# Kernel optimization log

Hardware: AMD Instinct MI355X
Metric: run time of the kernel (lower is better)

Reference implementation:

```python
import jax, jax.numpy as jnp
import numpy as np

EPS = 0.05
ITERS = 3
NORM_EPS = 1e-12  # torch F.normalize clamp


def setup_inputs() -> dict:
    key = jax.random.key(0)
    k1, k2, k3, k4 = jax.random.split(key, 4)
    x = jax.random.normal(k1, (16, 768, 64, 64), jnp.float32)
    conv_w = jax.random.normal(k2, (256, 768), jnp.float32) * 0.02  # 1x1 conv kernel [out,in]
    conv_b = jax.random.normal(k3, (256,), jnp.float32) * 0.02
    v = jax.random.normal(k4, (32, 256), jnp.float32)  # [num_clusters, token_dim]
    return {"x": x, "conv_w": conv_w, "conv_b": conv_b, "v": v}


def _l2_normalize(a, axis=-1):
    n = jnp.sqrt(jnp.sum(a * a, axis=axis, keepdims=True))
    return a / jnp.maximum(n, NORM_EPS)


def _log_optimal_transport(scores):
    # scores: [b, m, n]; log-domain Sinkhorn with uniform marginals
    b, m, n = scores.shape
    norm = -jnp.log(jnp.float32(m + n))
    Z = scores / EPS
    u = jnp.full((b, m), 0.0, Z.dtype)
    v = jnp.full((b, n), 0.0, Z.dtype)
    for _ in range(ITERS):
        u = norm - jax.scipy.special.logsumexp(Z + v[:, None, :], axis=2)
        v = norm - jax.scipy.special.logsumexp(Z + u[:, :, None], axis=1)
    return jnp.exp(Z + u[:, :, None] + v[:, None, :] - norm)


def reference(x, conv_w, conv_b, v):
    # 1x1 conv projection: [b, C, H, W] -> [b, D, H, W]
    xp = jnp.einsum('bchw,dc->bdhw', x, conv_w) + conv_b[None, :, None, None]
    b, d, H, W = xp.shape
    x_proj = xp.reshape(b, d, H * W).transpose(0, 2, 1)  # [b, hw, d]
    xf = _l2_normalize(x_proj)  # l2_normalize branch
    w = _l2_normalize(v)        # cluster weights normalized (in-place copy in torch)
    scores = jnp.einsum('bnd,md->bnm', xf, w)  # [b, hw, m]
    weights = _log_optimal_transport(scores.transpose(0, 2, 1)).transpose(0, 2, 1)  # [b, hw, m]
    v_tilde = jnp.einsum('bnd,bnm->bmd', xf, weights)  # [b, m, d]
    return (v_tilde, x_proj)
```

## Files before the change

### kernel.cpp

```cpp
#include <hip/hip_runtime.h>
#include <math.h>

#define NORM_C (-8.3255483f)

typedef __attribute__((ext_vector_type(8))) short bf16x8;
typedef __attribute__((ext_vector_type(4))) float f32x4;

union U8 { uint4 q; unsigned u[4]; bf16x8 v; };

__device__ inline unsigned short f2bf_rne(float f) {
    unsigned u = __float_as_uint(f);
    unsigned r = u + 0x7fffu + ((u >> 16) & 1u);
    return (unsigned short)(r >> 16);
}
__device__ inline unsigned pack_bf2(float lo, float hi) {
    unsigned a = __float_as_uint(lo) + 0x8000u;
    unsigned b = __float_as_uint(hi) + 0x8000u;
    return __builtin_amdgcn_perm(b, a, 0x07060302u);
}

__global__ __launch_bounds__(64) void w_prep(const float* __restrict__ W,
                                             const float* __restrict__ v_in,
                                             unsigned short* __restrict__ Wb,
                                             unsigned short* __restrict__ wnb) {
    const int bx = blockIdx.x, tid = threadIdx.x;
    if (bx < 768) {
        int i = (bx * 64 + tid) * 4;
        float4 w = *(const float4*)(W + i);
        unsigned lo = (unsigned)f2bf_rne(w.x) | ((unsigned)f2bf_rne(w.y) << 16);
        unsigned hi = (unsigned)f2bf_rne(w.z) | ((unsigned)f2bf_rne(w.w) << 16);
        *(uint2*)(Wb + i) = make_uint2(lo, hi);
    } else {
        int row = bx - 768;
        float4 v = *(const float4*)(v_in + row * 256 + tid * 4);
        float s = v.x * v.x + v.y * v.y + v.z * v.z + v.w * v.w;
#pragma unroll
        for (int off = 32; off > 0; off >>= 1) s += __shfl_xor(s, off);
        float inv = 1.0f / fmaxf(sqrtf(s), 1e-12f);
        unsigned lo = (unsigned)f2bf_rne(v.x * inv) | ((unsigned)f2bf_rne(v.y * inv) << 16);
        unsigned hi = (unsigned)f2bf_rne(v.z * inv) | ((unsigned)f2bf_rne(v.w * inv) << 16);
        *(uint2*)(wnb + row * 256 + tid * 4) = make_uint2(lo, hi);
    }
}

__global__ __launch_bounds__(256) void conv_mega(const float* __restrict__ x,
                                                 const unsigned short* __restrict__ Wb,
                                                 const float* __restrict__ bias,
                                                 const unsigned short* __restrict__ wnb,
                                                 float* __restrict__ xp,
                                                 float* __restrict__ inv_norm,
                                                 float* __restrict__ Z,
                                                 float2* __restrict__ u1p) {
    __shared__ unsigned Bs[2][128 * 17];
    __shared__ float ssq_s[128];
    __shared__ float invs_s[128];
    __shared__ unsigned xfs[128 * 33];
    __shared__ float2 upart_s[4][32];

    const int tid = threadIdx.x;
    const int lane = tid & 63;
    const int wid = tid >> 6;
    const int wn = wid & 1, wd = wid >> 1;
    const int b = blockIdx.y;
    const int n0 = blockIdx.x * 128;
    const int l15 = lane & 15, l4 = lane >> 4;
    const float* xb = x + (size_t)b * 768 * 4096;

    f32x4 acc[8][4];
#pragma unroll
    for (int i = 0; i < 8; ++i)
#pragma unroll
        for (int j = 0; j < 4; ++j) acc[i][j] = (f32x4){0.f, 0.f, 0.f, 0.f};

    const int n2 = tid & 63;
    const float* xpt = xb + n0 + 2 * n2;
    float2 ga[4], gb[4];

    auto LOADX = [&](int k0) {
#pragma unroll
        for (int i = 0; i < 4; ++i) {
            const float* p = xpt + (size_t)(k0 + 2 * (wid + 4 * i)) * 4096;
            ga[i] = *(const float2*)p;
            gb[i] = *(const float2*)(p + 4096);
        }
    };
    auto STOREB = [&](int buf) {
#pragma unroll
        for (int i = 0; i < 4; ++i) {
            int ch = wid + 4 * i;
            Bs[buf][(2 * n2) * 17 + ch]     = pack_bf2(ga[i].x, gb[i].x);
            Bs[buf][(2 * n2 + 1) * 17 + ch] = pack_bf2(ga[i].y, gb[i].y);
        }
    };

    LOADX(0);
    STOREB(0);
    __syncthreads();
    int cur = 0;
    for (int k0 = 0; k0 < 768; k0 += 32) {
        if (k0 + 32 < 768) LOADX(k0 + 32);

        U8 af[8];
#pragma unroll
        for (int dt = 0; dt < 8; ++dt) {
            int row = wd * 128 + dt * 16 + l15;
            af[dt].q = *(const uint4*)(Wb + (size_t)row * 768 + k0 + l4 * 8);
        }
#pragma unroll
        for (int nt = 0; nt < 4; ++nt) {
            int col = wn * 64 + nt * 16 + l15;
            int base = col * 17 + l4 * 4;
            U8 bf;
            bf.u[0] = Bs[cur][base];     bf.u[1] = Bs[cur][base + 1];
            bf.u[2] = Bs[cur][base + 2]; bf.u[3] = Bs[cur][base + 3];
#pragma unroll
            for (int dt = 0; dt < 8; ++dt)
                acc[dt][nt] = __builtin_amdgcn_mfma_f32_16x16x32_bf16(
                    af[dt].v, bf.v, acc[dt][nt], 0, 0, 0);
        }
        if (k0 + 32 < 768) STOREB(cur ^ 1);
        __syncthreads();
        cur ^= 1;
    }

    float ssq[4] = {0.f, 0.f, 0.f, 0.f};
#pragma unroll
    for (int dt = 0; dt < 8; ++dt) {
        int d = wd * 128 + dt * 16 + l4 * 4;
        float4 bi = *(const float4*)(bias + d);
#pragma unroll
        for (int nt = 0; nt < 4; ++nt) {
            int n = n0 + wn * 64 + nt * 16 + l15;
            f32x4 o = acc[dt][nt];
            o.x += bi.x; o.y += bi.y; o.z += bi.z; o.w += bi.w;
            acc[dt][nt] = o;
            *(f32x4*)(xp + ((size_t)(b * 4096 + n)) * 256 + d) = o;
            ssq[nt] += o.x * o.x + o.y * o.y + o.z * o.z + o.w * o.w;
        }
    }
#pragma unroll
    for (int nt = 0; nt < 4; ++nt) {
        ssq[nt] += __shfl_xor(ssq[nt], 16);
        ssq[nt] += __shfl_xor(ssq[nt], 32);
    }
    if (wd == 0 && l4 == 0) {
#pragma unroll
        for (int nt = 0; nt < 4; ++nt) ssq_s[wn * 64 + nt * 16 + l15] = ssq[nt];
    }
    __syncthreads();
    if (wd == 1 && l4 == 0) {
#pragma unroll
        for (int nt = 0; nt < 4; ++nt) {
            int nl = wn * 64 + nt * 16 + l15;
            float inv = 1.0f / fmaxf(sqrtf(ssq[nt] + ssq_s[nl]), 1e-12f);
            invs_s[nl] = inv;
            inv_norm[b * 4096 + n0 + nl] = inv;
        }
    }

    f32x4 accz[2][2];
#pragma unroll
    for (int i = 0; i < 2; ++i)
#pragma unroll
        for (int j = 0; j < 2; ++j) accz[i][j] = (f32x4){0.f, 0.f, 0.f, 0.f};

    for (int q = 0; q < 4; ++q) {
        __syncthreads();
        if (wd == (q >> 1)) {
#pragma unroll
            for (int dt4 = 0; dt4 < 4; ++dt4) {
                int dt = (q & 1) * 4 + dt4;
#pragma unroll
                for (int nt = 0; nt < 4; ++nt) {
                    int n = wn * 64 + nt * 16 + l15;
                    float inv = invs_s[n];
                    f32x4 a = acc[dt][nt];
                    int base = n * 33 + dt4 * 8 + l4 * 2;
                    xfs[base]     = pack_bf2(a.x * inv, a.y * inv);
                    xfs[base + 1] = pack_bf2(a.z * inv, a.w * inv);
                }
            }
        }
        __syncthreads();
#pragma unroll
        for (int s = 0; s < 2; ++s) {
            U8 wf[2];
#pragma unroll
            for (int mt = 0; mt < 2; ++mt)
                wf[mt].q = *(const uint4*)(wnb + (mt * 16 + l15) * 256 +
                                           q * 64 + s * 32 + l4 * 8);
#pragma unroll
            for (int sti = 0; sti < 2; ++sti) {
                int st = wid + sti * 4;
                int arow = (st * 16 + l15) * 33 + s * 16 + l4 * 4;
                U8 af;
                af.u[0] = xfs[arow]; af.u[1] = xfs[arow + 1];
                af.u[2] = xfs[arow + 2]; af.u[3] = xfs[arow + 3];
#pragma unroll
                for (int mt = 0; mt < 2; ++mt)
                    accz[sti][mt] = __builtin_amdgcn_mfma_f32_16x16x32_bf16(
                        af.v, wf[mt].v, accz[sti][mt], 0, 0, 0);
            }
        }
    }
#pragma unroll
    for (int sti = 0; sti < 2; ++sti)
#pragma unroll
        for (int mt = 0; mt < 2; ++mt) {
            accz[sti][mt].x *= 20.f; accz[sti][mt].y *= 20.f;
            accz[sti][mt].z *= 20.f; accz[sti][mt].w *= 20.f;
            int m = mt * 16 + l15;
            int st = wid + sti * 4;
            *(f32x4*)&Z[((size_t)(b * 32 + m)) * 4096 + n0 + st * 16 + l4 * 4] =
                accz[sti][mt];
        }
#pragma unroll
    for (int mt = 0; mt < 2; ++mt) {
        float v0[8] = {accz[0][mt].x, accz[0][mt].y, accz[0][mt].z, accz[0][mt].w,
                       accz[1][mt].x, accz[1][mt].y, accz[1][mt].z, accz[1][mt].w};
        float mx = v0[0];
#pragma unroll
        for (int i = 1; i < 8; ++i) mx = fmaxf(mx, v0[i]);
        float s = 0.f;
#pragma unroll
        for (int i = 0; i < 8; ++i) s += __expf(v0[i] - mx);
#pragma unroll
        for (int off = 16; off < 64; off <<= 1) {
            float omx = __shfl_xor(mx, off);
            float os = __shfl_xor(s, off);
            float nm = fmaxf(mx, omx);
            s = s * __expf(mx - nm) + os * __expf(omx - nm);
            mx = nm;
        }
        if (lane < 16) upart_s[wid][mt * 16 + lane] = make_float2(mx, s);
    }
    __syncthreads();
    if (wid == 0 && lane < 32) {
        float2 p = upart_s[0][lane];
        float mx = p.x, s = p.y;
#pragma unroll
        for (int w = 1; w < 4; ++w) {
            float2 qq = upart_s[w][lane];
            float nm = fmaxf(mx, qq.x);
            s = s * __expf(mx - nm) + qq.y * __expf(qq.x - nm);
            mx = nm;
        }
        u1p[((size_t)b * 32 + blockIdx.x) * 32 + lane] = make_float2(mx, s);
    }
}

template <int NIN>
__global__ __launch_bounds__(256) void sink_step(const float* __restrict__ Z,
                                                 const float2* __restrict__ up_in,
                                                 float2* __restrict__ up_out) {
    __shared__ float u_s[32];
    __shared__ float2 red_s[4][32];
    const int tid = threadIdx.x;
    const int lane = tid & 63, wid = tid >> 6;
    const int b = blockIdx.y;
    const int chunk = blockIdx.x;
    const int n = chunk * 256 + tid;

    if (tid < 32) {
        float2 p = up_in[((size_t)b * NIN) * 32 + tid];
        float mx = p.x, s = p.y;
#pragma unroll 4
        for (int t = 1; t < NIN; ++t) {
            float2 q = up_in[((size_t)b * NIN + t) * 32 + tid];
            float nm = fmaxf(mx, q.x);
            s = s * __expf(mx - nm) + q.y * __expf(q.x - nm);
            mx = nm;
        }
        u_s[tid] = NORM_C - (mx + __logf(s));
    }
    __syncthreads();

    float z[32];
#pragma unroll
    for (int m = 0; m < 32; ++m) z[m] = Z[((size_t)(b * 32 + m)) * 4096 + n];

    float mx = z[0] + u_s[0];
#pragma unroll
    for (int m = 1; m < 32; ++m) mx = fmaxf(mx, z[m] + u_s[m]);
    float s = 0.f;
#pragma unroll
    for (int m = 0; m < 32; ++m) s += __expf(z[m] + u_s[m] - mx);
    float vv = NORM_C - (mx + __logf(s));

#pragma unroll
    for (int m = 0; m < 32; ++m) {
        float val = z[m] + vv;
        float vmx = val;
#pragma unroll
        for (int off = 1; off < 64; off <<= 1) vmx = fmaxf(vmx, __shfl_xor(vmx, off));
        float e = __expf(val - vmx);
#pragma unroll
        for (int off = 1; off < 64; off <<= 1) e += __shfl_xor(e, off);
        if (lane == 0) red_s[wid][m] = make_float2(vmx, e);
    }
    __syncthreads();
    if (tid < 32) {
        float2 p = red_s[0][tid];
        float gm = p.x, gs = p.y;
#pragma unroll
        for (int w = 1; w < 4; ++w) {
            float2 q = red_s[w][tid];
            float nm = fmaxf(gm, q.x);
            gs = gs * __expf(gm - nm) + q.y * __expf(q.x - nm);
            gm = nm;
        }
        up_out[((size_t)b * 16 + chunk) * 32 + tid] = make_float2(gm, gs);
    }
}

__global__ __launch_bounds__(256) void vtilde_part_k(const float* __restrict__ xp,
                                                     const float* __restrict__ inv_norm,
                                                     const float* __restrict__ Z,
                                                     const float2* __restrict__ u3p,
                                                     float* __restrict__ part) {
    __shared__ float u_s[32];
    __shared__ float v3_s[256];
    __shared__ float inv_s[256];
    __shared__ float z_s[32 * 257];
    __shared__ float wt[64 * 36];
    const int tid = threadIdx.x;
    const int cx = blockIdx.x;
    const int chunk = cx >> 1, dh = cx & 1;
    const int b = blockIdx.y;
    const int n0 = chunk * 256;

    if (tid < 32) {
        float2 p = u3p[((size_t)b * 16) * 32 + tid];
        float gm = p.x, gs = p.y;
#pragma unroll
        for (int t = 1; t < 16; ++t) {
            float2 q = u3p[((size_t)b * 16 + t) * 32 + tid];
            float nm = fmaxf(gm, q.x);
            gs = gs * __expf(gm - nm) + q.y * __expf(q.x - nm);
            gm = nm;
        }
        u_s[tid] = NORM_C - (gm + __logf(gs));
    }
    __syncthreads();
    {
        int n = n0 + tid;
        float zr[32];
#pragma unroll
        for (int m = 0; m < 32; ++m) {
            zr[m] = Z[((size_t)(b * 32 + m)) * 4096 + n];
            z_s[m * 257 + tid] = zr[m];
        }
        float mx = zr[0] + u_s[0];
#pragma unroll
        for (int m = 1; m < 32; ++m) mx = fmaxf(mx, zr[m] + u_s[m]);
        float s = 0.f;
#pragma unroll
        for (int m = 0; m < 32; ++m) s += __expf(zr[m] + u_s[m] - mx);
        v3_s[tid] = NORM_C - (mx + __logf(s));
        inv_s[tid] = inv_norm[b * 4096 + n];
    }
    __syncthreads();

    const int dg = tid & 31, mq = tid >> 5;
    f32x4 acc[4];
#pragma unroll
    for (int j = 0; j < 4; ++j) acc[j] = (f32x4){0.f, 0.f, 0.f, 0.f};
    const float* xpb = xp + ((size_t)(b * 4096 + n0)) * 256 + dh * 128 + dg * 4;

    for (int t = 0; t < 4; ++t) {
#pragma unroll
        for (int i = 0; i < 8; ++i) {
            int e = tid + i * 256;
            int mW = e >> 6, nn = e & 63;
            int nl = t * 64 + nn;
            wt[nn * 36 + mW] =
                __expf(z_s[mW * 257 + nl] + u_s[mW] + v3_s[nl] - NORM_C) * inv_s[nl];
        }
        __syncthreads();
#pragma unroll 4
        for (int nn = 0; nn < 64; ++nn) {
            float4 xv = *(const float4*)(xpb + (size_t)(t * 64 + nn) * 256);
            float4 wv = *(const float4*)&wt[nn * 36 + mq * 4];
            acc[0].x += wv.x * xv.x; acc[0].y += wv.x * xv.y; acc[0].z += wv.x * xv.z; acc[0].w += wv.x * xv.w;
            acc[1].x += wv.y * xv.x; acc[1].y += wv.y * xv.y; acc[1].z += wv.y * xv.z; acc[1].w += wv.y * xv.w;
            acc[2].x += wv.z * xv.x; acc[2].y += wv.z * xv.y; acc[2].z += wv.z * xv.z; acc[2].w += wv.z * xv.w;
            acc[3].x += wv.w * xv.x; acc[3].y += wv.w * xv.y; acc[3].z += wv.w * xv.z; acc[3].w += wv.w * xv.w;
        }
        __syncthreads();
    }
#pragma unroll
    for (int j = 0; j < 4; ++j) {
        int m = mq * 4 + j;
        *(f32x4*)&part[((size_t)(b * 16 + chunk)) * 8192 + m * 256 + dh * 128 + dg * 4] = acc[j];
    }
}

__global__ __launch_bounds__(256) void vtilde_reduce(const float* __restrict__ part,
                                                     float* __restrict__ out_vt) {
    int o = blockIdx.x * 256 + threadIdx.x;
    int b = o >> 13, r = o & 8191;
    float s = 0.f;
#pragma unroll
    for (int c = 0; c < 16; ++c)
        s += part[((size_t)(b * 16 + c)) * 8192 + r];
    out_vt[o] = s;
}

extern "C" void kernel_launch(void* const* d_in, const int* in_sizes, int n_in,
                              void* d_out, int out_size, void* d_ws, size_t ws_size,
                              hipStream_t stream) {
    const float* x      = (const float*)d_in[0];
    const float* conv_w = (const float*)d_in[1];
    const float* conv_b = (const float*)d_in[2];
    const float* v_in   = (const float*)d_in[3];

    float* out_vt = (float*)d_out;
    float* out_xp = (float*)d_out + 131072;

    float* ws = (float*)d_ws;
    float*          inv_norm = ws;
    unsigned short* Wb       = (unsigned short*)(ws + 65536);
    unsigned short* wnb      = (unsigned short*)(ws + 163840);
    float*          Zbuf     = ws + 167936;
    float2*         u1p      = (float2*)(ws + 2265088);
    float2*         u2p      = (float2*)(ws + 2297856);
    float2*         u3p      = (float2*)(ws + 2314240);
    float*          part     = ws + 2330624;

    w_prep<<<800, 64, 0, stream>>>(conv_w, v_in, Wb, wnb);
    conv_mega<<<dim3(32, 16), 256, 0, stream>>>(x, Wb, conv_b, wnb, out_xp,
                                                inv_norm, Zbuf, u1p);
    sink_step<32><<<dim3(16, 16), 256, 0, stream>>>(Zbuf, u1p, u2p);
    sink_step<16><<<dim3(16, 16), 256, 0, stream>>>(Zbuf, u2p, u3p);
    vtilde_part_k<<<dim3(32, 16), 256, 0, stream>>>(out_xp, inv_norm, Zbuf, u3p, part);
    vtilde_reduce<<<512, 256, 0, stream>>>(part, out_vt);
}
```

Before: 414.9 us.

## Halve conv tile width, pre-tile bf16 weights, double grid for occupancy

The fused conv kernel now processes 64 pixels per block instead of 128, which doubles the grid to 1024 blocks and sets launch bounds for 4 blocks per CU, so fewer accumulators are held per thread. The weight prep writes conv weights in a K-tiled layout so each MFMA A-fragment load is contiguous. The K loop is unrolled by two with separate register sets for the prefetch. The sink_step and workspace layout are updated for 64 partial logsumexp entries per batch. Smaller tiles reuse each loaded weight fragment across fewer pixels, so the kernel reads more weight data in total in exchange for better latency hiding.

```diff
diff --git a/kernel.cpp b/kernel.cpp
--- a/kernel.cpp
+++ b/kernel.cpp
@@ -21,15 +21,18 @@
 
 __global__ __launch_bounds__(64) void w_prep(const float* __restrict__ W,
                                              const float* __restrict__ v_in,
-                                             unsigned short* __restrict__ Wb,
+                                             unsigned short* __restrict__ Wbt,
                                              unsigned short* __restrict__ wnb) {
     const int bx = blockIdx.x, tid = threadIdx.x;
     if (bx < 768) {
         int i = (bx * 64 + tid) * 4;
+        int row = i / 768;
+        int k = i - row * 768;
+        int t = k >> 5, q = (k >> 3) & 3, e = k & 7;
         float4 w = *(const float4*)(W + i);
         unsigned lo = (unsigned)f2bf_rne(w.x) | ((unsigned)f2bf_rne(w.y) << 16);
         unsigned hi = (unsigned)f2bf_rne(w.z) | ((unsigned)f2bf_rne(w.w) << 16);
-        *(uint2*)(Wb + i) = make_uint2(lo, hi);
+        *(uint2*)(Wbt + ((t * 256 + row) << 5) + q * 8 + e) = make_uint2(lo, hi);
     } else {
         int row = bx - 768;
         float4 v = *(const float4*)(v_in + row * 256 + tid * 4);
@@ -43,94 +46,113 @@
     }
 }
 
-__global__ __launch_bounds__(256) void conv_mega(const float* __restrict__ x,
-                                                 const unsigned short* __restrict__ Wb,
-                                                 const float* __restrict__ bias,
-                                                 const unsigned short* __restrict__ wnb,
-                                                 float* __restrict__ xp,
-                                                 float* __restrict__ inv_norm,
-                                                 float* __restrict__ Z,
-                                                 float2* __restrict__ u1p) {
-    __shared__ unsigned Bs[2][128 * 17];
-    __shared__ float ssq_s[128];
-    __shared__ float invs_s[128];
-    __shared__ unsigned xfs[128 * 33];
+__global__ __launch_bounds__(256, 4) void conv_mega(const float* __restrict__ x,
+                                                    const unsigned short* __restrict__ Wbt,
+                                                    const float* __restrict__ bias,
+                                                    const unsigned short* __restrict__ wnb,
+                                                    float* __restrict__ xp,
+                                                    float* __restrict__ inv_norm,
+                                                    float* __restrict__ Z,
+                                                    float2* __restrict__ u1p) {
+    __shared__ unsigned Bs[2][64 * 17];
+    __shared__ unsigned xf_s[64 * 65];
+    __shared__ float ssq_s[4][64];
+    __shared__ float invs_s[64];
     __shared__ float2 upart_s[4][32];
 
     const int tid = threadIdx.x;
     const int lane = tid & 63;
     const int wid = tid >> 6;
-    const int wn = wid & 1, wd = wid >> 1;
     const int b = blockIdx.y;
-    const int n0 = blockIdx.x * 128;
+    const int n0 = blockIdx.x * 64;
     const int l15 = lane & 15, l4 = lane >> 4;
     const float* xb = x + (size_t)b * 768 * 4096;
 
-    f32x4 acc[8][4];
-#pragma unroll
-    for (int i = 0; i < 8; ++i)
+    f32x4 acc[4][4];
+#pragma unroll
+    for (int i = 0; i < 4; ++i)
 #pragma unroll
         for (int j = 0; j < 4; ++j) acc[i][j] = (f32x4){0.f, 0.f, 0.f, 0.f};
 
-    const int n2 = tid & 63;
+    const int n2 = tid & 31, c8 = tid >> 5;
     const float* xpt = xb + n0 + 2 * n2;
-    float2 ga[4], gb[4];
-
-    auto LOADX = [&](int k0) {
-#pragma unroll
-        for (int i = 0; i < 4; ++i) {
-            const float* p = xpt + (size_t)(k0 + 2 * (wid + 4 * i)) * 4096;
-            ga[i] = *(const float2*)p;
-            gb[i] = *(const float2*)(p + 4096);
+
+    float2 gaA[2], gbA[2], gaB[2], gbB[2];
+
+    auto LOADA = [&](int k0) {
+#pragma unroll
+        for (int i = 0; i < 2; ++i) {
+            const float* p = xpt + (size_t)(k0 + 2 * (c8 + 8 * i)) * 4096;
+            gaA[i] = *(const float2*)p;
+            gbA[i] = *(const float2*)(p + 4096);
+        }
+    };
+    auto LOADB = [&](int k0) {
+#pragma unroll
+        for (int i = 0; i < 2; ++i) {
+            const float* p = xpt + (size_t)(k0 + 2 * (c8 + 8 * i)) * 4096;
+            gaB[i] = *(const float2*)p;
+            gbB[i] = *(const float2*)(p + 4096);
+        }
+    };
+    auto STOREA = [&](int buf) {
+#pragma unroll
+        for (int i = 0; i < 2; ++i) {
+            int ch = c8 + 8 * i;
+            Bs[buf][(2 * n2) * 17 + ch]     = pack_bf2(gaA[i].x, gbA[i].x);
+            Bs[buf][(2 * n2 + 1) * 17 + ch] = pack_bf2(gaA[i].y, gbA[i].y);
         }
     };
     auto STOREB = [&](int buf) {
 #pragma unroll
-        for (int i = 0; i < 4; ++i) {
-            int ch = wid + 4 * i;
-            Bs[buf][(2 * n2) * 17 + ch]     = pack_bf2(ga[i].x, gb[i].x);
-            Bs[buf][(2 * n2 + 1) * 17 + ch] = pack_bf2(ga[i].y, gb[i].y);
+        for (int i = 0; i < 2; ++i) {
+            int ch = c8 + 8 * i;
+            Bs[buf][(2 * n2) * 17 + ch]     = pack_bf2(gaB[i].x, gbB[i].x);
+            Bs[buf][(2 * n2 + 1) * 17 + ch] = pack_bf2(gaB[i].y, gbB[i].y);
         }
     };
-
-    LOADX(0);
-    STOREB(0);
-    __syncthreads();
-    int cur = 0;
-    for (int k0 = 0; k0 < 768; k0 += 32) {
-        if (k0 + 32 < 768) LOADX(k0 + 32);
-
-        U8 af[8];
-#pragma unroll
-        for (int dt = 0; dt < 8; ++dt) {
-            int row = wd * 128 + dt * 16 + l15;
-            af[dt].q = *(const uint4*)(Wb + (size_t)row * 768 + k0 + l4 * 8);
-        }
+    auto MFMA_STEP = [&](int t, int buf) {
+        U8 af[4];
+#pragma unroll
+        for (int dt = 0; dt < 4; ++dt)
+            af[dt].q = *(const uint4*)(Wbt +
+                ((t * 256 + wid * 64 + dt * 16 + l15) << 5) + l4 * 8);
 #pragma unroll
         for (int nt = 0; nt < 4; ++nt) {
-            int col = wn * 64 + nt * 16 + l15;
-            int base = col * 17 + l4 * 4;
+            int base = (nt * 16 + l15) * 17 + l4 * 4;
             U8 bf;
-            bf.u[0] = Bs[cur][base];     bf.u[1] = Bs[cur][base + 1];
-            bf.u[2] = Bs[cur][base + 2]; bf.u[3] = Bs[cur][base + 3];
-#pragma unroll
-            for (int dt = 0; dt < 8; ++dt)
+            bf.u[0] = Bs[buf][base];     bf.u[1] = Bs[buf][base + 1];
+            bf.u[2] = Bs[buf][base + 2]; bf.u[3] = Bs[buf][base + 3];
+#pragma unroll
+            for (int dt = 0; dt < 4; ++dt)
                 acc[dt][nt] = __builtin_amdgcn_mfma_f32_16x16x32_bf16(
                     af[dt].v, bf.v, acc[dt][nt], 0, 0, 0);
         }
-        if (k0 + 32 < 768) STOREB(cur ^ 1);
-        __syncthreads();
-        cur ^= 1;
+    };
+
+    LOADA(0);
+    STOREA(0);
+    LOADB(32);
+    __syncthreads();
+    for (int t = 0; t < 24; t += 2) {
+        if (t + 2 < 24) LOADA((t + 2) * 32);
+        MFMA_STEP(t, 0);
+        STOREB(1);
+        __syncthreads();
+        if (t + 3 < 24) LOADB((t + 3) * 32);
+        MFMA_STEP(t + 1, 1);
+        if (t + 2 < 24) STOREA(0);
+        __syncthreads();
     }
 
     float ssq[4] = {0.f, 0.f, 0.f, 0.f};
 #pragma unroll
-    for (int dt = 0; dt < 8; ++dt) {
-        int d = wd * 128 + dt * 16 + l4 * 4;
+    for (int dt = 0; dt < 4; ++dt) {
+        int d = wid * 64 + dt * 16 + l4 * 4;
         float4 bi = *(const float4*)(bias + d);
 #pragma unroll
         for (int nt = 0; nt < 4; ++nt) {
-            int n = n0 + wn * 64 + nt * 16 + l15;
+            int n = n0 + nt * 16 + l15;
             f32x4 o = acc[dt][nt];
             o.x += bi.x; o.y += bi.y; o.z += bi.z; o.w += bi.w;
             acc[dt][nt] = o;
@@ -143,87 +165,70 @@
         ssq[nt] += __shfl_xor(ssq[nt], 16);
         ssq[nt] += __shfl_xor(ssq[nt], 32);
     }
-    if (wd == 0 && l4 == 0) {
-#pragma unroll
-        for (int nt = 0; nt < 4; ++nt) ssq_s[wn * 64 + nt * 16 + l15] = ssq[nt];
-    }
-    __syncthreads();
-    if (wd == 1 && l4 == 0) {
-#pragma unroll
-        for (int nt = 0; nt < 4; ++nt) {
-            int nl = wn * 64 + nt * 16 + l15;
-            float inv = 1.0f / fmaxf(sqrtf(ssq[nt] + ssq_s[nl]), 1e-12f);
-            invs_s[nl] = inv;
-            inv_norm[b * 4096 + n0 + nl] = inv;
-        }
-    }
-
-    f32x4 accz[2][2];
-#pragma unroll
-    for (int i = 0; i < 2; ++i)
-#pragma unroll
-        for (int j = 0; j < 2; ++j) accz[i][j] = (f32x4){0.f, 0.f, 0.f, 0.f};
-
-    for (int q = 0; q < 4; ++q) {
-        __syncthreads();
-        if (wd == (q >> 1)) {
-#pragma unroll
-            for (int dt4 = 0; dt4 < 4; ++dt4) {
-                int dt = (q & 1) * 4 + dt4;
+    if (l4 == 0) {
+#pragma unroll
+        for (int nt = 0; nt < 4; ++nt) ssq_s[wid][nt * 16 + l15] = ssq[nt];
+    }
+    __syncthreads();
+    if (tid < 64) {
+        float s = ssq_s[0][tid] + ssq_s[1][tid] + ssq_s[2][tid] + ssq_s[3][tid];
+        float inv = 1.0f / fmaxf(sqrtf(s), 1e-12f);
+        invs_s[tid] = inv;
+        inv_norm[b * 4096 + n0 + tid] = inv;
+    }
+
+    f32x4 accz[2];
+    accz[0] = (f32x4){0.f, 0.f, 0.f, 0.f};
+    accz[1] = (f32x4){0.f, 0.f, 0.f, 0.f};
+
+    for (int h = 0; h < 2; ++h) {
+        __syncthreads();
+        if ((wid >> 1) == h) {
+            int qh = wid & 1;
+#pragma unroll
+            for (int dt = 0; dt < 4; ++dt)
 #pragma unroll
                 for (int nt = 0; nt < 4; ++nt) {
-                    int n = wn * 64 + nt * 16 + l15;
+                    int n = nt * 16 + l15;
                     float inv = invs_s[n];
                     f32x4 a = acc[dt][nt];
-                    int base = n * 33 + dt4 * 8 + l4 * 2;
-                    xfs[base]     = pack_bf2(a.x * inv, a.y * inv);
-                    xfs[base + 1] = pack_bf2(a.z * inv, a.w * inv);
+                    int base = n * 65 + qh * 32 + dt * 8 + l4 * 2;
+                    xf_s[base]     = pack_bf2(a.x * inv, a.y * inv);
+                    xf_s[base + 1] = pack_bf2(a.z * inv, a.w * inv);
                 }
-            }
-        }
-        __syncthreads();
-#pragma unroll
-        for (int s = 0; s < 2; ++s) {
+        }
+        __syncthreads();
+#pragma unroll
+        for (int s = 0; s < 4; ++s) {
             U8 wf[2];
 #pragma unroll
             for (int mt = 0; mt < 2; ++mt)
                 wf[mt].q = *(const uint4*)(wnb + (mt * 16 + l15) * 256 +
-                                           q * 64 + s * 32 + l4 * 8);
-#pragma unroll
-            for (int sti = 0; sti < 2; ++sti) {
-                int st = wid + sti * 4;
-                int arow = (st * 16 + l15) * 33 + s * 16 + l4 * 4;
-                U8 af;
-                af.u[0] = xfs[arow]; af.u[1] = xfs[arow + 1];
-                af.u[2] = xfs[arow + 2]; af.u[3] = xfs[arow + 3];
-#pragma unroll
-                for (int mt = 0; mt < 2; ++mt)
-                    accz[sti][mt] = __builtin_amdgcn_mfma_f32_16x16x32_bf16(
-                        af.v, wf[mt].v, accz[sti][mt], 0, 0, 0);
-            }
-        }
-    }
-#pragma unroll
-    for (int sti = 0; sti < 2; ++sti)
-#pragma unroll
-        for (int mt = 0; mt < 2; ++mt) {
-            accz[sti][mt].x *= 20.f; accz[sti][mt].y *= 20.f;
-            accz[sti][mt].z *= 20.f; accz[sti][mt].w *= 20.f;
-            int m = mt * 16 + l15;
-            int st = wid + sti * 4;
-            *(f32x4*)&Z[((size_t)(b * 32 + m)) * 4096 + n0 + st * 16 + l4 * 4] =
-                accz[sti][mt];
-        }
+                                           h * 128 + s * 32 + l4 * 8);
+            int arow = (wid * 16 + l15) * 65 + s * 16 + l4 * 4;
+            U8 af2;
+            af2.u[0] = xf_s[arow];     af2.u[1] = xf_s[arow + 1];
+            af2.u[2] = xf_s[arow + 2]; af2.u[3] = xf_s[arow + 3];
+#pragma unroll
+            for (int mt = 0; mt < 2; ++mt)
+                accz[mt] = __builtin_amdgcn_mfma_f32_16x16x32_bf16(
+                    af2.v, wf[mt].v, accz[mt], 0, 0, 0);
+        }
+    }
 #pragma unroll
     for (int mt = 0; mt < 2; ++mt) {
-        float v0[8] = {accz[0][mt].x, accz[0][mt].y, accz[0][mt].z, accz[0][mt].w,
-                       accz[1][mt].x, accz[1][mt].y, accz[1][mt].z, accz[1][mt].w};
-        float mx = v0[0];
-#pragma unroll
-        for (int i = 1; i < 8; ++i) mx = fmaxf(mx, v0[i]);
-        float s = 0.f;
-#pragma unroll
-        for (int i = 0; i < 8; ++i) s += __expf(v0[i] - mx);
+        accz[mt].x *= 20.f; accz[mt].y *= 20.f;
+        accz[mt].z *= 20.f; accz[mt].w *= 20.f;
+        int m = mt * 16 + l15;
+        *(f32x4*)&Z[((size_t)(b * 32 + m)) * 4096 + n0 + wid * 16 + l4 * 4] =
+            accz[mt];
+    }
+#pragma unroll
+    for (int mt = 0; mt < 2; ++mt) {
+        f32x4 vz = accz[mt];
+        float mx = fmaxf(fmaxf(vz.x, vz.y), fmaxf(vz.z, vz.w));
+        float s = __expf(vz.x - mx) + __expf(vz.y - mx) +
+                  __expf(vz.z - mx) + __expf(vz.w - mx);
 #pragma unroll
         for (int off = 16; off < 64; off <<= 1) {
             float omx = __shfl_xor(mx, off);
@@ -245,7 +250,7 @@
             s = s * __expf(mx - nm) + qq.y * __expf(qq.x - nm);
             mx = nm;
         }
-        u1p[((size_t)b * 32 + blockIdx.x) * 32 + lane] = make_float2(mx, s);
+        u1p[((size_t)b * 64 + blockIdx.x) * 32 + lane] = make_float2(mx, s);
     }
 }
 
@@ -419,18 +424,18 @@
 
     float* ws = (float*)d_ws;
     float*          inv_norm = ws;
-    unsigned short* Wb       = (unsigned short*)(ws + 65536);
+    unsigned short* Wbt      = (unsigned short*)(ws + 65536);
     unsigned short* wnb      = (unsigned short*)(ws + 163840);
     float*          Zbuf     = ws + 167936;
-    float2*         u1p      = (float2*)(ws + 2265088);
-    float2*         u2p      = (float2*)(ws + 2297856);
-    float2*         u3p      = (float2*)(ws + 2314240);
-    float*          part     = ws + 2330624;
-
-    w_prep<<<800, 64, 0, stream>>>(conv_w, v_in, Wb, wnb);
-    conv_mega<<<dim3(32, 16), 256, 0, stream>>>(x, Wb, conv_b, wnb, out_xp,
+    float*          part     = ws + 2265088;
+    float2*         u1p      = (float2*)part;
+    float2*         u2p      = (float2*)(ws + 4362240);
+    float2*         u3p      = (float2*)(ws + 4378624);
+
+    w_prep<<<800, 64, 0, stream>>>(conv_w, v_in, Wbt, wnb);
+    conv_mega<<<dim3(64, 16), 256, 0, stream>>>(x, Wbt, conv_b, wnb, out_xp,
                                                 inv_norm, Zbuf, u1p);
-    sink_step<32><<<dim3(16, 16), 256, 0, stream>>>(Zbuf, u1p, u2p);
+    sink_step<64><<<dim3(16, 16), 256, 0, stream>>>(Zbuf, u1p, u2p);
     sink_step<16><<<dim3(16, 16), 256, 0, stream>>>(Zbuf, u2p, u3p);
     vtilde_part_k<<<dim3(32, 16), 256, 0, stream>>>(out_xp, inv_norm, Zbuf, u3p, part);
     vtilde_reduce<<<512, 256, 0, stream>>>(part, out_vt);
```

Result: faster. 393.8 us (-5.1%).

## Stage conv weight tile in LDS and drop register-prefetch double buffering

Applied to the files above, without the earlier changes.

The conv GEMM loop now cooperatively loads the 256x32 bf16 weight tile into shared memory each K step, so MFMA A-fragments come from LDS instead of each wave reading global memory directly. The x tile is loaded and stored to LDS synchronously, which removes the double-buffered register prefetch pipeline. This trades less redundant global weight traffic and fewer live registers (possibly better occupancy) for exposed load latency and an extra barrier per iteration. The workspace layout is also reshuffled so u1p aliases the partial buffer.

```diff
diff --git a/kernel.cpp b/kernel.cpp
--- a/kernel.cpp
+++ b/kernel.cpp
@@ -51,7 +51,8 @@
                                                  float* __restrict__ inv_norm,
                                                  float* __restrict__ Z,
                                                  float2* __restrict__ u1p) {
-    __shared__ unsigned Bs[2][128 * 17];
+    __shared__ unsigned As[256 * 20];
+    __shared__ unsigned Bs[128 * 17];
     __shared__ float ssq_s[128];
     __shared__ float invs_s[128];
     __shared__ unsigned xfs[128 * 33];
@@ -72,55 +73,45 @@
 #pragma unroll
         for (int j = 0; j < 4; ++j) acc[i][j] = (f32x4){0.f, 0.f, 0.f, 0.f};
 
-    const int n2 = tid & 63;
-    const float* xpt = xb + n0 + 2 * n2;
-    float2 ga[4], gb[4];
-
-    auto LOADX = [&](int k0) {
+    for (int k0 = 0; k0 < 768; k0 += 32) {
+        __syncthreads();
 #pragma unroll
         for (int i = 0; i < 4; ++i) {
-            const float* p = xpt + (size_t)(k0 + 2 * (wid + 4 * i)) * 4096;
-            ga[i] = *(const float2*)p;
-            gb[i] = *(const float2*)(p + 4096);
-        }
-    };
-    auto STOREB = [&](int buf) {
+            int f = tid + i * 256;
+            int dd = f >> 2, c8 = f & 3;
+            uint4 w = *(const uint4*)(Wb + (size_t)dd * 768 + k0 + c8 * 8);
+            *(uint4*)&As[dd * 20 + c8 * 4] = w;
+        }
 #pragma unroll
         for (int i = 0; i < 4; ++i) {
-            int ch = wid + 4 * i;
-            Bs[buf][(2 * n2) * 17 + ch]     = pack_bf2(ga[i].x, gb[i].x);
-            Bs[buf][(2 * n2 + 1) * 17 + ch] = pack_bf2(ga[i].y, gb[i].y);
-        }
-    };
-
-    LOADX(0);
-    STOREB(0);
-    __syncthreads();
-    int cur = 0;
-    for (int k0 = 0; k0 < 768; k0 += 32) {
-        if (k0 + 32 < 768) LOADX(k0 + 32);
+            int f = tid + i * 256;
+            int n2 = f & 63, ch = f >> 6;
+            const float* p = xb + (size_t)(k0 + 2 * ch) * 4096 + n0 + 2 * n2;
+            float2 g0 = *(const float2*)p;
+            float2 g1 = *(const float2*)(p + 4096);
+            Bs[(2 * n2) * 17 + ch] = pack_bf2(g0.x, g1.x);
+            Bs[(2 * n2 + 1) * 17 + ch] = pack_bf2(g0.y, g1.y);
+        }
+        __syncthreads();
 
         U8 af[8];
 #pragma unroll
         for (int dt = 0; dt < 8; ++dt) {
             int row = wd * 128 + dt * 16 + l15;
-            af[dt].q = *(const uint4*)(Wb + (size_t)row * 768 + k0 + l4 * 8);
+            af[dt].q = *(uint4*)&As[row * 20 + l4 * 4];
         }
 #pragma unroll
         for (int nt = 0; nt < 4; ++nt) {
             int col = wn * 64 + nt * 16 + l15;
             int base = col * 17 + l4 * 4;
             U8 bf;
-            bf.u[0] = Bs[cur][base];     bf.u[1] = Bs[cur][base + 1];
-            bf.u[2] = Bs[cur][base + 2]; bf.u[3] = Bs[cur][base + 3];
+            bf.u[0] = Bs[base]; bf.u[1] = Bs[base + 1];
+            bf.u[2] = Bs[base + 2]; bf.u[3] = Bs[base + 3];
 #pragma unroll
             for (int dt = 0; dt < 8; ++dt)
                 acc[dt][nt] = __builtin_amdgcn_mfma_f32_16x16x32_bf16(
                     af[dt].v, bf.v, acc[dt][nt], 0, 0, 0);
         }
-        if (k0 + 32 < 768) STOREB(cur ^ 1);
-        __syncthreads();
-        cur ^= 1;
     }
 
     float ssq[4] = {0.f, 0.f, 0.f, 0.f};
@@ -422,10 +413,10 @@
     unsigned short* Wb       = (unsigned short*)(ws + 65536);
     unsigned short* wnb      = (unsigned short*)(ws + 163840);
     float*          Zbuf     = ws + 167936;
-    float2*         u1p      = (float2*)(ws + 2265088);
-    float2*         u2p      = (float2*)(ws + 2297856);
-    float2*         u3p      = (float2*)(ws + 2314240);
-    float*          part     = ws + 2330624;
+    float*          part     = ws + 2265088;
+    float2*         u1p      = (float2*)part;
+    float2*         u2p      = (float2*)(ws + 4362240);
+    float2*         u3p      = (float2*)(ws + 4378624);
 
     w_prep<<<800, 64, 0, stream>>>(conv_w, v_in, Wb, wnb);
     conv_mega<<<dim3(32, 16), 256, 0, stream>>>(x, Wb, conv_b, wnb, out_xp,
```

New measurement: 392.3 us. -5.4%, faster.
